# Kernel optimization log

Measured on AMD Instinct MI355X. Metric: run time of the kernel, lower is better.

Reference implementation:

```python
import jax, jax.numpy as jnp
import numpy as np

Z, H, W = 8, 96, 192
WZ, WH, WW = 2, 6, 12
C, HEADS, DEPTH, B = 192, 6, 2, 1
NZ, NH, NW = Z // WZ, H // WH, W // WW
LW = WZ * WH * WW            # 144 tokens per window
WIN_TYPES = NZ * NH          # 64 earth-specific window types
NPOS = WZ * WZ * WH * WH * (2 * WW - 1)  # 3312 relative-position entries
HD = C // HEADS
SCALE = HD ** -0.5
SZ, SH, SW = WZ // 2, WH // 2, WW // 2


def _position_index():
    czi = np.arange(WZ); czj = -np.arange(WZ) * WZ
    chi = np.arange(WH); chj = -np.arange(WH) * WH
    cw = np.arange(WW)
    c1 = np.stack(np.meshgrid(czi, chi, cw, indexing='ij'), 0).reshape(3, -1)
    c2 = np.stack(np.meshgrid(czj, chj, cw, indexing='ij'), 0).reshape(3, -1)
    coords = (c1[:, :, None] - c2[:, None, :]).transpose(1, 2, 0).astype(np.int64).copy()
    coords[:, :, 2] += WW - 1
    coords[:, :, 1] *= 2 * WW - 1
    coords[:, :, 0] *= (2 * WW - 1) * WH * WH
    return coords.sum(-1).reshape(-1)


def _attention_mask():
    m = np.zeros((Z, H, W))
    zs = (slice(0, -WZ), slice(-WZ, -SZ), slice(-SZ, None))
    hs = (slice(0, -WH), slice(-WH, -SH), slice(-SH, None))
    ws = (slice(0, -WW), slice(-WW, -SW), slice(-SW, None))
    cnt = 0
    for z in zs:
        for h in hs:
            for w in ws:
                m[z, h, w] = cnt
                cnt += 1
    mw = m.reshape(NZ, WZ, NH, WH, NW, WW).transpose(0, 2, 4, 1, 3, 5).reshape(-1, LW)
    d = mw[:, None, :] - mw[:, :, None]
    return np.where(d != 0, -100.0, 0.0).astype(np.float32)


def setup_inputs() -> dict:
    key = jax.random.key(0)
    ks = jax.random.split(key, 12)
    s = 0.02
    def rn(k, shape):
        return jax.random.normal(k, shape, jnp.float32) * s
    return {
        'x': jax.random.normal(ks[0], (B, Z * H * W, C), jnp.float32),
        'qkv_w': rn(ks[1], (DEPTH, C, 3 * C)),
        'qkv_b': rn(ks[2], (DEPTH, 3 * C)),
        'proj_w': rn(ks[3], (DEPTH, C, C)),
        'proj_b': rn(ks[4], (DEPTH, C)),
        'bias_tab': rn(ks[5], (DEPTH, NPOS, WIN_TYPES, HEADS)),
        'n1_g': jnp.ones((DEPTH, C), jnp.float32),
        'n1_b': jnp.zeros((DEPTH, C), jnp.float32),
        'n2_g': jnp.ones((DEPTH, C), jnp.float32),
        'n2_b': jnp.zeros((DEPTH, C), jnp.float32),
        'mlp_w1': rn(ks[6], (DEPTH, C, 4 * C)),
        'mlp_b1': rn(ks[7], (DEPTH, 4 * C)),
        'mlp_w2': rn(ks[8], (DEPTH, 4 * C, C)),
        'mlp_b2': rn(ks[9], (DEPTH, C)),
        'pos_index': jnp.asarray(_position_index(), jnp.int32),
        'attn_mask': jnp.asarray(_attention_mask()),
    }


def _ln(x, g, b):
    m = x.mean(-1, keepdims=True)
    v = jnp.mean((x - m) ** 2, -1, keepdims=True)
    return (x - m) / jnp.sqrt(v + 1e-5) * g + b


def _forward(x, qkv_w, qkv_b, proj_w, proj_b, bias_tab, n1_g, n1_b, n2_g, n2_b,
             mlp_w1, mlp_b1, mlp_w2, mlp_b2, pos_index, attn_mask):
    for blk in range(DEPTH):
        roll = (blk % 2 == 1)
        shortcut = x
        h = _ln(x, n1_g[blk], n1_b[blk]).reshape(B, Z, H, W, C)
        if roll:
            h = jnp.roll(h, (-SZ, -SH, -SW), (1, 2, 3))
        # partition windows: (B*nZ*nH*nW, LW, C)
        h = h.reshape(B, NZ, WZ, NH, WH, NW, WW, C).transpose(0, 1, 3, 5, 2, 4, 6, 7).reshape(-1, LW, C)
        B_ = h.shape[0]
        qkv = (h @ qkv_w[blk] + qkv_b[blk]).reshape(B_, LW, 3, HEADS, HD)
        q = qkv[:, :, 0].transpose(0, 2, 1, 3) * SCALE  # (B_, heads, LW, hd)
        k = qkv[:, :, 1].transpose(0, 2, 1, 3)
        v = qkv[:, :, 2].transpose(0, 2, 1, 3)
        attn = jnp.einsum('bhid,bhjd->bhij', q, k)
        # earth-specific bias gathered by relative-position index
        bias = bias_tab[blk][pos_index].reshape(LW, LW, WIN_TYPES, HEADS).transpose(2, 3, 0, 1)
        attn = (attn.reshape(-1, WIN_TYPES, HEADS, LW, LW) + bias).reshape(B_, HEADS, LW, LW)
        if roll:
            attn = (attn.reshape(B, WIN_TYPES * NW, HEADS, LW, LW) + attn_mask[None, :, None]).reshape(B_, HEADS, LW, LW)
        attn = jax.nn.softmax(attn, -1)
        o = jnp.einsum('bhij,bhjd->bhid', attn, v).transpose(0, 2, 1, 3).reshape(B_, LW, C)
        o = o @ proj_w[blk] + proj_b[blk]
        # reverse windows
        o = o.reshape(B, NZ, NH, NW, WZ, WH, WW, C).transpose(0, 1, 4, 2, 5, 3, 6, 7).reshape(B, Z, H, W, C)
        if roll:
            o = jnp.roll(o, (SZ, SH, SW), (1, 2, 3))
        x = shortcut + o.reshape(B, Z * H * W, C)
        h2 = _ln(x, n2_g[blk], n2_b[blk])
        h2 = jax.nn.gelu(h2 @ mlp_w1[blk] + mlp_b1[blk], approximate=False) @ mlp_w2[blk] + mlp_b2[blk]
        x = x + h2
    return x


def reference(x, qkv_w, qkv_b, proj_w, proj_b, bias_tab, n1_g, n1_b, n2_g, n2_b,
              mlp_w1, mlp_b1, mlp_w2, mlp_b2, pos_index, attn_mask):
    return _forward(x, qkv_w, qkv_b, proj_w, proj_b, bias_tab, n1_g, n1_b, n2_g, n2_b,
                    mlp_w1, mlp_b1, mlp_w2, mlp_b2, pos_index, attn_mask)
```

## Files before the change

kernel.cpp:

```cpp
#include <hip/hip_runtime.h>
#include <math.h>

#define TZ 8
#define TH 96
#define TW 192
#define C 192
#define NHEADS 6
#define HDIM 32
#define LW 144
#define NWIN 1024
#define NTOK 147456
#define NPOS 3312
#define QSCALE 0.17677669529663687f

typedef unsigned short u16;
typedef __attribute__((ext_vector_type(8))) short bf8_t;
typedef __attribute__((ext_vector_type(4))) float f4_t;

__device__ __forceinline__ float bf2f(u16 u) {
    union { unsigned int i; float f; } c; c.i = ((unsigned int)u) << 16; return c.f;
}
__device__ __forceinline__ u16 f2bf(float f) {
    union { float f; unsigned int i; } c; c.f = f;
    unsigned int x = c.i;
    x += 0x7fffu + ((x >> 16) & 1u);
    return (u16)(x >> 16);
}

__device__ __forceinline__ int win_row_to_token(int r, int roll) {
    int wi = r / LW, l = r % LW;
    int nz = wi >> 8, nh = (wi >> 4) & 15, nw = wi & 15;
    int iz = l / 72, rr = l % 72, ih = rr / 12, iw = rr % 12;
    int z = nz * 2 + iz, h = nh * 6 + ih, w = nw * 12 + iw;
    if (roll) {
        z = (z + 1) & 7;
        h += 3; if (h >= TH) h -= TH;
        w += 6; if (w >= TW) w -= TW;
    }
    return (z * TH + h) * TW + w;
}

__global__ __launch_bounds__(256) void ln_kernel(
    const float* __restrict__ x, const float* __restrict__ g,
    const float* __restrict__ b, u16* __restrict__ xnc,
    int row0, int windowed, int roll)
{
    int wave = threadIdx.x >> 6;
    int lane = threadIdx.x & 63;
    int dl = blockIdx.x * 4 + wave;
    int d = row0 + dl;
    int src = windowed ? win_row_to_token(d, roll) : d;
    const float* xr = x + (size_t)src * C;
    float v0 = xr[lane], v1 = xr[lane + 64], v2 = xr[lane + 128];
    float s = v0 + v1 + v2;
    float sq = v0 * v0 + v1 * v1 + v2 * v2;
    #pragma unroll
    for (int off = 32; off > 0; off >>= 1) {
        s  += __shfl_xor(s, off, 64);
        sq += __shfl_xor(sq, off, 64);
    }
    float mean = s * (1.0f / 192.0f);
    float var  = sq * (1.0f / 192.0f) - mean * mean;
    float rstd = rsqrtf(var + 1e-5f);
    u16* orow = xnc + (size_t)dl * C;
    orow[lane]       = f2bf((v0 - mean) * rstd * g[lane]       + b[lane]);
    orow[lane + 64]  = f2bf((v1 - mean) * rstd * g[lane + 64]  + b[lane + 64]);
    orow[lane + 128] = f2bf((v2 - mean) * rstd * g[lane + 128] + b[lane + 128]);
}

__global__ __launch_bounds__(256) void tconv_kernel(
    const float* __restrict__ W, u16* __restrict__ WT, int K, int N)
{
    int idx = blockIdx.x * 256 + threadIdx.x;
    if (idx >= N * K) return;
    int n = idx / K, k = idx % K;
    WT[idx] = f2bf(W[(size_t)k * N + n]);
}

__global__ __launch_bounds__(256) void biasmat_kernel(
    const float* __restrict__ btab, const int* __restrict__ pidx,
    u16* __restrict__ biasf)
{
    int wt = blockIdx.x, head = blockIdx.y;
    size_t obase = ((size_t)wt * 6 + head) * (LW * LW);
    for (int idx = threadIdx.x; idx < LW * LW; idx += 256) {
        int p = pidx[idx];
        biasf[obase + idx] = f2bf(btab[((size_t)p * 64 + wt) * 6 + head]);
    }
}

template <int MODE>
__global__ __launch_bounds__(256) void mm_kernel(
    const u16* __restrict__ A, const u16* __restrict__ BT,
    const float* __restrict__ bias, void* __restrict__ Cvoid,
    int N, int K, int row0, int roll)
{
    __shared__ alignas(16) u16 As[128 * 72];
    __shared__ alignas(16) u16 Bs[64 * 72];
    int tid = threadIdx.x;
    int mb = blockIdx.y * 128, nb = blockIdx.x * 64;
    int wave = tid >> 6, lane = tid & 63;
    int mh = wave >> 1, nh = wave & 1;
    int lr = lane & 15, g = lane >> 4;

    f4_t acc[4][2];
    #pragma unroll
    for (int mi = 0; mi < 4; mi++)
        #pragma unroll
        for (int ni = 0; ni < 2; ni++)
            acc[mi][ni] = (f4_t){0.f, 0.f, 0.f, 0.f};

    for (int k0 = 0; k0 < K; k0 += 64) {
        #pragma unroll
        for (int it = 0; it < 4; it++) {
            int idx = it * 256 + tid;
            int r = idx >> 3, kc = idx & 7;
            *(bf8_t*)&As[r * 72 + kc * 8] =
                *(const bf8_t*)&A[(size_t)(mb + r) * K + k0 + kc * 8];
        }
        #pragma unroll
        for (int it = 0; it < 2; it++) {
            int idx = it * 256 + tid;
            int r = idx >> 3, kc = idx & 7;
            *(bf8_t*)&Bs[r * 72 + kc * 8] =
                *(const bf8_t*)&BT[(size_t)(nb + r) * K + k0 + kc * 8];
        }
        __syncthreads();
        #pragma unroll
        for (int ks = 0; ks < 2; ks++) {
            bf8_t bfr[2];
            #pragma unroll
            for (int ni = 0; ni < 2; ni++)
                bfr[ni] = *(const bf8_t*)&Bs[(nh * 32 + ni * 16 + lr) * 72 + ks * 32 + g * 8];
            #pragma unroll
            for (int mi = 0; mi < 4; mi++) {
                bf8_t afr = *(const bf8_t*)&As[(mh * 64 + mi * 16 + lr) * 72 + ks * 32 + g * 8];
                #pragma unroll
                for (int ni = 0; ni < 2; ni++)
                    acc[mi][ni] = __builtin_amdgcn_mfma_f32_16x16x32_bf16(
                        afr, bfr[ni], acc[mi][ni], 0, 0, 0);
            }
        }
        __syncthreads();
    }

    #pragma unroll
    for (int mi = 0; mi < 4; mi++) {
        int rbase = mb + mh * 64 + mi * 16 + g * 4;
        int tok[4];
        if (MODE == 1) {
            #pragma unroll
            for (int r = 0; r < 4; r++)
                tok[r] = win_row_to_token(row0 + rbase + r, roll);
        }
        #pragma unroll
        for (int ni = 0; ni < 2; ni++) {
            int col = nb + nh * 32 + ni * 16 + lr;
            float bb = bias[col];
            #pragma unroll
            for (int r = 0; r < 4; r++) {
                float v = acc[mi][ni][r] + bb;
                if (MODE == 0) {
                    if (col < 192) v *= QSCALE;
                    ((u16*)Cvoid)[(size_t)(rbase + r) * 576 + col] = f2bf(v);
                } else if (MODE == 1) {
                    ((float*)Cvoid)[(size_t)tok[r] * C + col] += v;
                } else if (MODE == 2) {
                    v = 0.5f * v * (1.0f + erff(v * 0.70710678118654752f));
                    ((u16*)Cvoid)[(size_t)(rbase + r) * 768 + col] = f2bf(v);
                } else {
                    ((float*)Cvoid)[(size_t)(row0 + rbase + r) * C + col] += v;
                }
            }
        }
    }
}

__global__ __launch_bounds__(192) void attn_kernel(
    const u16* __restrict__ qkvb, const u16* __restrict__ biasf,
    u16* __restrict__ attnb, int win0, int roll)
{
    __shared__ alignas(16) u16 Qs[144 * 40];
    __shared__ alignas(16) u16 Ks[144 * 40];
    __shared__ alignas(16) u16 Vt[32 * 168];
    __shared__ alignas(16) u16 Ps[3 * 16 * 168];
    __shared__ int region[144];

    int wl = blockIdx.x, head = blockIdx.y;
    int wi = win0 + wl, wt = wi & 63;
    int tid = threadIdx.x;

    const u16* base = qkvb + (size_t)wl * LW * 576;
    for (int idx = tid; idx < 144 * 32; idx += 192) {
        int l = idx >> 5, d = idx & 31;
        const u16* row = base + (size_t)l * 576 + head * 32;
        Qs[l * 40 + d] = row[d];
        Ks[l * 40 + d] = row[192 + d];
        Vt[d * 168 + l] = row[384 + d];
    }
    for (int idx = tid; idx < 32 * 24; idx += 192) {
        int d = idx / 24, c2 = 144 + idx % 24;
        Vt[d * 168 + c2] = 0;
    }
    for (int idx = tid; idx < 48 * 24; idx += 192) {
        int rw = idx / 24, c2 = 144 + idx % 24;
        Ps[rw * 168 + c2] = 0;
    }
    if (tid < 144) {
        int nz = wi >> 8, nh = (wi >> 4) & 15, nw = wi & 15;
        int iz = tid / 72, rr = tid % 72, ih = rr / 12, iw = rr % 12;
        int z = nz * 2 + iz, h = nh * 6 + ih, w = nw * 12 + iw;
        int rz = (z < 6) ? 0 : ((z < 7) ? 1 : 2);
        int rh = (h < 90) ? 0 : ((h < 93) ? 1 : 2);
        int rw2 = (w < 180) ? 0 : ((w < 186) ? 1 : 2);
        region[tid] = rz * 9 + rh * 3 + rw2;
    }
    __syncthreads();

    int wave = tid >> 6, lane = tid & 63;
    int lr = lane & 15, g = lane >> 4;
    u16* Pbuf = &Ps[wave * 16 * 168];

    for (int itl = 0; itl < 3; itl++) {
        int it = wave * 3 + itl;
        bf8_t aQ = *(const bf8_t*)&Qs[(it * 16 + lr) * 40 + g * 8];
        f4_t s[9];
        #pragma unroll
        for (int jt = 0; jt < 9; jt++) {
            bf8_t bK = *(const bf8_t*)&Ks[(jt * 16 + lr) * 40 + g * 8];
            f4_t z4 = {0.f, 0.f, 0.f, 0.f};
            s[jt] = __builtin_amdgcn_mfma_f32_16x16x32_bf16(aQ, bK, z4, 0, 0, 0);
        }
        int rowbase = it * 16 + g * 4;
        const u16* bb = biasf + ((size_t)(wt * 6 + head) * LW + rowbase) * LW + lr;
        int regRow[4], regCol[9];
        if (roll) {
            #pragma unroll
            for (int r = 0; r < 4; r++) regRow[r] = region[rowbase + r];
            #pragma unroll
            for (int jt = 0; jt < 9; jt++) regCol[jt] = region[jt * 16 + lr];
        }
        float m4[4] = {-1e30f, -1e30f, -1e30f, -1e30f};
        #pragma unroll
        for (int jt = 0; jt < 9; jt++)
            #pragma unroll
            for (int r = 0; r < 4; r++) {
                float v = s[jt][r] + bf2f(bb[r * LW + jt * 16]);
                if (roll && (regCol[jt] != regRow[r])) v -= 100.0f;
                s[jt][r] = v;
                m4[r] = fmaxf(m4[r], v);
            }
        #pragma unroll
        for (int off = 1; off < 16; off <<= 1)
            #pragma unroll
            for (int r = 0; r < 4; r++)
                m4[r] = fmaxf(m4[r], __shfl_xor(m4[r], off, 64));
        float l4[4] = {0.f, 0.f, 0.f, 0.f};
        #pragma unroll
        for (int jt = 0; jt < 9; jt++)
            #pragma unroll
            for (int r = 0; r < 4; r++) {
                float p = __expf(s[jt][r] - m4[r]);
                s[jt][r] = p;
                l4[r] += p;
            }
        #pragma unroll
        for (int off = 1; off < 16; off <<= 1)
            #pragma unroll
            for (int r = 0; r < 4; r++)
                l4[r] += __shfl_xor(l4[r], off, 64);
        float inv4[4];
        #pragma unroll
        for (int r = 0; r < 4; r++) inv4[r] = 1.0f / l4[r];

        __syncthreads();
        #pragma unroll
        for (int jt = 0; jt < 9; jt++)
            #pragma unroll
            for (int r = 0; r < 4; r++)
                Pbuf[(g * 4 + r) * 168 + jt * 16 + lr] = f2bf(s[jt][r] * inv4[r]);
        __syncthreads();

        #pragma unroll
        for (int dt = 0; dt < 2; dt++) {
            f4_t acc = {0.f, 0.f, 0.f, 0.f};
            #pragma unroll
            for (int kt = 0; kt < 5; kt++) {
                bf8_t aP = *(const bf8_t*)&Pbuf[lr * 168 + kt * 32 + g * 8];
                bf8_t bV = *(const bf8_t*)&Vt[(dt * 16 + lr) * 168 + kt * 32 + g * 8];
                acc = __builtin_amdgcn_mfma_f32_16x16x32_bf16(aP, bV, acc, 0, 0, 0);
            }
            #pragma unroll
            for (int r = 0; r < 4; r++)
                attnb[(size_t)(wl * LW + rowbase + r) * 192 + head * 32 + dt * 16 + lr]
                    = f2bf(acc[r]);
        }
    }
}

extern "C" void kernel_launch(void* const* d_in, const int* in_sizes, int n_in,
                              void* d_out, int out_size, void* d_ws, size_t ws_size,
                              hipStream_t stream)
{
    (void)in_sizes; (void)n_in; (void)out_size; (void)ws_size;
    const float* x_in   = (const float*)d_in[0];
    const float* qkv_w  = (const float*)d_in[1];
    const float* qkv_b  = (const float*)d_in[2];
    const float* proj_w = (const float*)d_in[3];
    const float* proj_b = (const float*)d_in[4];
    const float* btab   = (const float*)d_in[5];
    const float* n1g    = (const float*)d_in[6];
    const float* n1b    = (const float*)d_in[7];
    const float* n2g    = (const float*)d_in[8];
    const float* n2b    = (const float*)d_in[9];
    const float* w1     = (const float*)d_in[10];
    const float* b1     = (const float*)d_in[11];
    const float* w2     = (const float*)d_in[12];
    const float* b2     = (const float*)d_in[13];
    const int*   pidx   = (const int*)d_in[14];

    float* x   = (float*)d_out;
    u16* biasf = (u16*)d_ws;
    u16* wT    = biasf + (size_t)64 * 6 * LW * LW;
    u16* xnc   = wT + 884736;
    u16* qkvb  = xnc + (size_t)NTOK * C;
    u16* attnb = qkvb + (size_t)NTOK * 576;
    u16* hidb  = qkvb;

    const size_t WBLK = 442368;
    const size_t OQKV = 0, OPROJ = 110592, OW1 = 147456, OW2 = 294912;

    hipMemcpyAsync(x, x_in, (size_t)NTOK * C * sizeof(float),
                   hipMemcpyDeviceToDevice, stream);

    for (int blk = 0; blk < 2; blk++) {
        u16* wb = wT + blk * WBLK;
        tconv_kernel<<<(576 * 192 + 255) / 256, 256, 0, stream>>>(
            qkv_w + (size_t)blk * C * 576, wb + OQKV, C, 576);
        tconv_kernel<<<(192 * 192 + 255) / 256, 256, 0, stream>>>(
            proj_w + (size_t)blk * C * C, wb + OPROJ, C, 192);
        tconv_kernel<<<(768 * 192 + 255) / 256, 256, 0, stream>>>(
            w1 + (size_t)blk * C * 768, wb + OW1, C, 768);
        tconv_kernel<<<(192 * 768 + 255) / 256, 256, 0, stream>>>(
            w2 + (size_t)blk * 768 * C, wb + OW2, 768, 192);
    }

    for (int blk = 0; blk < 2; blk++) {
        int roll = blk & 1;
        u16* wb = wT + blk * WBLK;
        biasmat_kernel<<<dim3(64, 6), 256, 0, stream>>>(
            btab + (size_t)blk * NPOS * 64 * 6, pidx, biasf);
        ln_kernel<<<NTOK / 4, 256, 0, stream>>>(
            x, n1g + blk * C, n1b + blk * C, xnc, 0, 1, roll);
        mm_kernel<0><<<dim3(9, NTOK / 128), 256, 0, stream>>>(
            xnc, wb + OQKV, qkv_b + blk * 576, qkvb, 576, C, 0, roll);
        attn_kernel<<<dim3(NWIN, NHEADS), 192, 0, stream>>>(
            qkvb, biasf, attnb, 0, roll);
        mm_kernel<1><<<dim3(3, NTOK / 128), 256, 0, stream>>>(
            attnb, wb + OPROJ, proj_b + blk * C, x, 192, C, 0, roll);
        ln_kernel<<<NTOK / 4, 256, 0, stream>>>(
            x, n2g + blk * C, n2b + blk * C, xnc, 0, 0, 0);
        mm_kernel<2><<<dim3(12, NTOK / 128), 256, 0, stream>>>(
            xnc, wb + OW1, b1 + blk * 768, hidb, 768, C, 0, 0);
        mm_kernel<3><<<dim3(3, NTOK / 128), 256, 0, stream>>>(
            hidb, wb + OW2, b2 + blk * C, x, 192, 768, 0, 0);
    }
}
```

Measured before the change: 1.582 ms.

## Keep softmax probabilities in registers via transposed MFMA in attention kernel

The attention kernel swaps the MFMA operand order so each lane owns one query row's scores. The P fragments can then feed the PV MFMA straight from registers, which removes the shared-memory P buffer and its two block-wide barriers per tile. Global loads of Q/K/V, bias reads and output stores become vectorized, row reductions need only two cross-lane shuffles, and the smaller LDS footprint plus a min-blocks launch bound is meant to raise occupancy. In exchange, the split K-dimension ordering across t/t+16 has to match the fragment layout exactly, and the V transpose store in the load loop is scalar.

Result: slower. 1.620 ms (+2.4%).

```diff
diff --git a/kernel.cpp b/kernel.cpp
--- a/kernel.cpp
+++ b/kernel.cpp
@@ -15,6 +15,8 @@
 
 typedef unsigned short u16;
 typedef __attribute__((ext_vector_type(8))) short bf8_t;
+typedef __attribute__((ext_vector_type(4))) short bf4_t;
+typedef __attribute__((ext_vector_type(4))) unsigned short us4_t;
 typedef __attribute__((ext_vector_type(4))) float f4_t;
 
 __device__ __forceinline__ float bf2f(u16 u) {
@@ -176,35 +178,29 @@
     }
 }
 
-__global__ __launch_bounds__(192) void attn_kernel(
+__global__ __launch_bounds__(192, 4) void attn_kernel(
     const u16* __restrict__ qkvb, const u16* __restrict__ biasf,
     u16* __restrict__ attnb, int win0, int roll)
 {
     __shared__ alignas(16) u16 Qs[144 * 40];
     __shared__ alignas(16) u16 Ks[144 * 40];
-    __shared__ alignas(16) u16 Vt[32 * 168];
-    __shared__ alignas(16) u16 Ps[3 * 16 * 168];
-    __shared__ int region[144];
+    __shared__ alignas(16) u16 Vt[32 * 148];
+    __shared__ unsigned char region8[144];
 
     int wl = blockIdx.x, head = blockIdx.y;
     int wi = win0 + wl, wt = wi & 63;
     int tid = threadIdx.x;
 
     const u16* base = qkvb + (size_t)wl * LW * 576;
-    for (int idx = tid; idx < 144 * 32; idx += 192) {
-        int l = idx >> 5, d = idx & 31;
+    for (int c = tid; c < 576; c += 192) {
+        int l = c >> 2, d8 = (c & 3) << 3;
         const u16* row = base + (size_t)l * 576 + head * 32;
-        Qs[l * 40 + d] = row[d];
-        Ks[l * 40 + d] = row[192 + d];
-        Vt[d * 168 + l] = row[384 + d];
-    }
-    for (int idx = tid; idx < 32 * 24; idx += 192) {
-        int d = idx / 24, c2 = 144 + idx % 24;
-        Vt[d * 168 + c2] = 0;
-    }
-    for (int idx = tid; idx < 48 * 24; idx += 192) {
-        int rw = idx / 24, c2 = 144 + idx % 24;
-        Ps[rw * 168 + c2] = 0;
+        *(bf8_t*)&Qs[l * 40 + d8] = *(const bf8_t*)&row[d8];
+        *(bf8_t*)&Ks[l * 40 + d8] = *(const bf8_t*)&row[192 + d8];
+        bf8_t v8 = *(const bf8_t*)&row[384 + d8];
+        #pragma unroll
+        for (int m = 0; m < 8; m++)
+            Vt[(d8 + m) * 148 + l] = (u16)v8[m];
     }
     if (tid < 144) {
         int nz = wi >> 8, nh = (wi >> 4) & 15, nw = wi & 15;
@@ -213,87 +209,98 @@
         int rz = (z < 6) ? 0 : ((z < 7) ? 1 : 2);
         int rh = (h < 90) ? 0 : ((h < 93) ? 1 : 2);
         int rw2 = (w < 180) ? 0 : ((w < 186) ? 1 : 2);
-        region[tid] = rz * 9 + rh * 3 + rw2;
+        region8[tid] = (unsigned char)(rz * 9 + rh * 3 + rw2);
     }
     __syncthreads();
 
     int wave = tid >> 6, lane = tid & 63;
     int lr = lane & 15, g = lane >> 4;
-    u16* Pbuf = &Ps[wave * 16 * 168];
+    int jb = g << 2;
+    const f4_t z4 = {0.f, 0.f, 0.f, 0.f};
 
     for (int itl = 0; itl < 3; itl++) {
         int it = wave * 3 + itl;
-        bf8_t aQ = *(const bf8_t*)&Qs[(it * 16 + lr) * 40 + g * 8];
+        int i_row = it * 16 + lr;
+        bf8_t qf = *(const bf8_t*)&Qs[i_row * 40 + (g << 3)];
         f4_t s[9];
         #pragma unroll
         for (int jt = 0; jt < 9; jt++) {
-            bf8_t bK = *(const bf8_t*)&Ks[(jt * 16 + lr) * 40 + g * 8];
-            f4_t z4 = {0.f, 0.f, 0.f, 0.f};
-            s[jt] = __builtin_amdgcn_mfma_f32_16x16x32_bf16(aQ, bK, z4, 0, 0, 0);
-        }
-        int rowbase = it * 16 + g * 4;
-        const u16* bb = biasf + ((size_t)(wt * 6 + head) * LW + rowbase) * LW + lr;
-        int regRow[4], regCol[9];
-        if (roll) {
-            #pragma unroll
-            for (int r = 0; r < 4; r++) regRow[r] = region[rowbase + r];
-            #pragma unroll
-            for (int jt = 0; jt < 9; jt++) regCol[jt] = region[jt * 16 + lr];
-        }
+            bf8_t kf = *(const bf8_t*)&Ks[(jt * 16 + lr) * 40 + (g << 3)];
+            s[jt] = __builtin_amdgcn_mfma_f32_16x16x32_bf16(kf, qf, z4, 0, 0, 0);
+        }
+
+        const u16* bb = biasf + ((size_t)(wt * 6 + head) * LW + i_row) * LW;
+        unsigned int ri = region8[i_row];
         float m4[4] = {-1e30f, -1e30f, -1e30f, -1e30f};
         #pragma unroll
-        for (int jt = 0; jt < 9; jt++)
+        for (int jt = 0; jt < 9; jt++) {
+            us4_t b4 = *(const us4_t*)&bb[jt * 16 + jb];
+            unsigned int rj = 0;
+            if (roll) rj = *(const unsigned int*)&region8[jt * 16 + jb];
             #pragma unroll
             for (int r = 0; r < 4; r++) {
-                float v = s[jt][r] + bf2f(bb[r * LW + jt * 16]);
-                if (roll && (regCol[jt] != regRow[r])) v -= 100.0f;
+                float v = s[jt][r] + bf2f(b4[r]);
+                if (roll && (((rj >> (8 * r)) & 255u) != ri)) v -= 100.0f;
                 s[jt][r] = v;
                 m4[r] = fmaxf(m4[r], v);
             }
-        #pragma unroll
-        for (int off = 1; off < 16; off <<= 1)
-            #pragma unroll
-            for (int r = 0; r < 4; r++)
-                m4[r] = fmaxf(m4[r], __shfl_xor(m4[r], off, 64));
+        }
+        float m = fmaxf(fmaxf(m4[0], m4[1]), fmaxf(m4[2], m4[3]));
+        m = fmaxf(m, __shfl_xor(m, 16, 64));
+        m = fmaxf(m, __shfl_xor(m, 32, 64));
+
         float l4[4] = {0.f, 0.f, 0.f, 0.f};
         #pragma unroll
         for (int jt = 0; jt < 9; jt++)
             #pragma unroll
             for (int r = 0; r < 4; r++) {
-                float p = __expf(s[jt][r] - m4[r]);
+                float p = __expf(s[jt][r] - m);
                 s[jt][r] = p;
                 l4[r] += p;
             }
-        #pragma unroll
-        for (int off = 1; off < 16; off <<= 1)
-            #pragma unroll
-            for (int r = 0; r < 4; r++)
-                l4[r] += __shfl_xor(l4[r], off, 64);
-        float inv4[4];
-        #pragma unroll
-        for (int r = 0; r < 4; r++) inv4[r] = 1.0f / l4[r];
-
-        __syncthreads();
-        #pragma unroll
-        for (int jt = 0; jt < 9; jt++)
-            #pragma unroll
-            for (int r = 0; r < 4; r++)
-                Pbuf[(g * 4 + r) * 168 + jt * 16 + lr] = f2bf(s[jt][r] * inv4[r]);
-        __syncthreads();
+        float lsum = (l4[0] + l4[1]) + (l4[2] + l4[3]);
+        lsum += __shfl_xor(lsum, 16, 64);
+        lsum += __shfl_xor(lsum, 32, 64);
+        float inv = 1.0f / lsum;
+
+        bf8_t pfrag[5];
+        #pragma unroll
+        for (int t = 0; t < 4; t++)
+            #pragma unroll
+            for (int m2 = 0; m2 < 4; m2++) {
+                pfrag[t][m2]     = (short)f2bf(s[2 * t][m2] * inv);
+                pfrag[t][4 + m2] = (short)f2bf(s[2 * t + 1][m2] * inv);
+            }
+        #pragma unroll
+        for (int m2 = 0; m2 < 4; m2++) {
+            pfrag[4][m2]     = (short)f2bf(s[8][m2] * inv);
+            pfrag[4][4 + m2] = 0;
+        }
 
         #pragma unroll
         for (int dt = 0; dt < 2; dt++) {
-            f4_t acc = {0.f, 0.f, 0.f, 0.f};
-            #pragma unroll
-            for (int kt = 0; kt < 5; kt++) {
-                bf8_t aP = *(const bf8_t*)&Pbuf[lr * 168 + kt * 32 + g * 8];
-                bf8_t bV = *(const bf8_t*)&Vt[(dt * 16 + lr) * 168 + kt * 32 + g * 8];
-                acc = __builtin_amdgcn_mfma_f32_16x16x32_bf16(aP, bV, acc, 0, 0, 0);
-            }
-            #pragma unroll
-            for (int r = 0; r < 4; r++)
-                attnb[(size_t)(wl * LW + rowbase + r) * 192 + head * 32 + dt * 16 + lr]
-                    = f2bf(acc[r]);
+            const u16* vrow = &Vt[(dt * 16 + lr) * 148];
+            f4_t acc = z4;
+            #pragma unroll
+            for (int t = 0; t < 5; t++) {
+                bf4_t va = *(const bf4_t*)&vrow[t * 32 + jb];
+                bf8_t af;
+                #pragma unroll
+                for (int m2 = 0; m2 < 4; m2++) af[m2] = va[m2];
+                if (t < 4) {
+                    bf4_t vb = *(const bf4_t*)&vrow[t * 32 + 16 + jb];
+                    #pragma unroll
+                    for (int m2 = 0; m2 < 4; m2++) af[4 + m2] = vb[m2];
+                } else {
+                    #pragma unroll
+                    for (int m2 = 0; m2 < 4; m2++) af[4 + m2] = 0;
+                }
+                acc = __builtin_amdgcn_mfma_f32_16x16x32_bf16(af, pfrag[t], acc, 0, 0, 0);
+            }
+            us4_t o;
+            #pragma unroll
+            for (int r = 0; r < 4; r++) o[r] = f2bf(acc[r]);
+            *(us4_t*)&attnb[((size_t)wl * LW + i_row) * 192 + head * 32 + dt * 16 + jb] = o;
         }
     }
 }
```
